# Performance work log

Measured on AMD Instinct MI355X. Metric: run time of the kernel, lower is better.

The kernel has to match this reference:

```python
import jax, jax.numpy as jnp
import numpy as np

NEG_VALUE = -1e7
EPS = 1e-13


def setup_inputs() -> dict:
    key = jax.random.key(0)
    k1, k2, k3, k4, k5 = jax.random.split(key, 5)
    B, C_L, Q_L, D2 = 32, 2048, 256, 256  # D2 = 2*model_dim
    context = jax.random.normal(k1, (B, C_L, D2), dtype=jnp.float32)
    query = jax.random.normal(k2, (B, Q_L, D2), dtype=jnp.float32)
    context_mask = (jax.random.uniform(k3, (B, C_L)) > 0.1).astype(jnp.float32)
    query_mask = (jax.random.uniform(k4, (B, Q_L)) > 0.1).astype(jnp.float32)
    # Linear(6*model_dim, 1, bias=False) weight, flattened to [3*D2]
    W = jax.random.normal(k5, (3 * D2,), dtype=jnp.float32) * 0.05
    return {"context": context, "context_mask": context_mask,
            "query": query, "query_mask": query_mask, "W": W}


def _masked_softmax(vector, mask):
    # claf / old-AllenNLP style: softmax(vector * mask) * mask, renormalized
    result = jax.nn.softmax(vector * mask, axis=-1) * mask
    return result / (result.sum(axis=-1, keepdims=True) + EPS)


def reference(context, context_mask, query, query_mask, W):
    c, q = context, query
    D2 = c.shape[-1]
    w_c, w_q, w_cq = W[:D2], W[D2:2 * D2], W[2 * D2:]
    # Decomposed similarity: S[b,i,j] = c_i.w_c + q_j.w_q + (c_i*q_j).w_cq
    # (same math as Linear over concat(c_aug, q_aug, c_aug*q_aug), no 6D blowup)
    S = (jnp.einsum('bcd,d->bc', c, w_c)[:, :, None]
         + jnp.einsum('bqd,d->bq', q, w_q)[:, None, :]
         + jnp.einsum('bcd,bqd->bcq', c * w_cq, q))  # [B, C_L, Q_L]

    qm = query_mask[:, None, :]  # [B, 1, Q_L]
    # add_masked_value: vector*mask + (1-mask)*value
    masked_S = S * qm + (1.0 - qm) * NEG_VALUE

    # C2Q: masked softmax over query dim, weighted sum of q
    attn_c2q = _masked_softmax(S, qm)                      # [B, C_L, Q_L]
    c2q = jnp.einsum('bcq,bqd->bcd', attn_c2q, q)           # [B, C_L, D2]

    # Q2C: max over query dim, masked softmax over context dim, weighted sum of c
    s_max = masked_S.max(axis=-1)                           # [B, C_L]
    attn_q2c = _masked_softmax(s_max, context_mask)         # [B, C_L]
    q2c = jnp.einsum('bc,bcd->bd', attn_q2c, c)             # [B, D2]

    G = jnp.concatenate(
        [c, c2q, c * c2q, c * q2c[:, None, :]], axis=-1)    # [B, C_L, 4*D2]
    return G
```

## Files before the change

### kernel.cpp

```cpp
#include <hip/hip_runtime.h>


#define CL 2048
#define QL 256
#define DD 256
#define TM 128
#define NEGV -1.0e7f

typedef short bs8 __attribute__((ext_vector_type(8)));
typedef float fx4 __attribute__((ext_vector_type(4)));

__device__ __forceinline__ short f2bf(float x) {
    unsigned u = __float_as_uint(x);
    unsigned r = (u + 0x7fffu + ((u >> 16) & 1u)) >> 16;
    return (short)r;
}
__device__ __forceinline__ float bf2f(short h) {
    return __uint_as_float(((unsigned)(unsigned short)h) << 16);
}
__device__ __forceinline__ void gl16(const short* g, short* l) {
    __builtin_amdgcn_global_load_lds(
        (const __attribute__((address_space(1))) void*)g,
        (__attribute__((address_space(3))) void*)l, 16, 0, 0);
}
#define LGKM0() asm volatile("s_waitcnt lgkmcnt(0)" ::: "memory")
#define VMC4()  asm volatile("s_waitcnt vmcnt(4)" ::: "memory")
#define VMC3()  asm volatile("s_waitcnt vmcnt(3)" ::: "memory")
#define VMC1()  asm volatile("s_waitcnt vmcnt(1)" ::: "memory")
#define VMC0()  asm volatile("s_waitcnt vmcnt(0)" ::: "memory")

__global__ void k0_split(const float* __restrict__ q, const float* __restrict__ W,
                         short* __restrict__ qh, short* __restrict__ qth,
                         float* __restrict__ sq) {
    __shared__ float lds[64][259];
    __shared__ float wq_l[256];
    int t = threadIdx.x, lane = t & 63, w = t >> 6;
    int b = blockIdx.y, cn = blockIdx.x;
    if (t < 64) *(fx4*)&wq_l[t * 4] = *(const fx4*)(W + 256 + t * 4);
    for (int r = 0; r < 64; ++r)
        lds[r][t] = q[((size_t)b * QL + cn * 64 + r) * DD + t];
    __syncthreads();
    for (int r = 0; r < 64; ++r) {
        size_t o = ((size_t)b * QL + cn * 64 + r) * DD + t;
        qh[o] = f2bf(lds[r][t]);
    }
    for (int dd = 0; dd < 64; ++dd) {
        int d = w * 64 + dd;
        size_t o = ((size_t)b * DD + d) * QL + cn * 64 + lane;
        qth[o] = f2bf(lds[lane][d]);
    }
    int r = t >> 2, qt = t & 3;
    float s = 0.0f;
    for (int i = 0; i < 64; ++i) {
        int colr = qt * 64 + ((i + r) & 63);
        s = fmaf(lds[r][colr], wq_l[colr], s);
    }
    s += __shfl_xor(s, 1, 64);
    s += __shfl_xor(s, 2, 64);
    if (qt == 0) sq[b * QL + cn * 64 + r] = s;
}

__global__ __launch_bounds__(1024, 4) void k1(
        const float* __restrict__ ctx, const float* __restrict__ qmask,
        const float* __restrict__ cmask,
        const short* __restrict__ qh, const short* __restrict__ qth,
        const float* __restrict__ sq, const float* __restrict__ W,
        float* __restrict__ G, float* __restrict__ q2cp,
        float* __restrict__ zup, float* __restrict__ zap) {
    __shared__ __align__(16) char SMEM[77312];
    short* Bc   = (short*)SMEM;
    short* Qt   = (short*)SMEM;
    float* pout = (float*)SMEM;
    short* Pb   = (short*)(SMEM + 32768);
    float* sq_l  = (float*)(SMEM + 67584);
    float* qm_l  = sq_l + 256;
    float* wcq_l = qm_l + 256;
    float* wc_l  = wcq_l + 256;
    float* sc_l  = wc_l + 256;
    float* redA  = sc_l + 128;
    float* redB  = redA + 512;
    float* er_l  = redB + 512;
    float* zar_l = er_l + 128;

    int t = threadIdx.x, lane = t & 63, wid = t >> 6;
    int wm = wid >> 1, wn = wid & 1;
    int l15 = lane & 15, lk = lane >> 4;
    int id = blockIdx.x;
    int xcd = id & 7, j = id >> 3;
    int b = xcd * 4 + (j >> 4);
    int bx = j & 15;
    int c0 = bx * TM;

    if (t < 256) sq_l[t] = sq[b * QL + t];
    else if (t < 512) qm_l[t - 256] = qmask[b * QL + (t - 256)];
    if (t < 64) *(fx4*)&wcq_l[t * 4] = *(const fx4*)(W + 512 + t * 4);
    else if (t < 128) *(fx4*)&wc_l[(t - 64) * 4] = *(const fx4*)(W + (t - 64) * 4);

    const short* qhb = qh + (size_t)b * QL * DD;
    const short* qtb = qth + (size_t)b * DD * QL;
    const float* ctxb = ctx + ((size_t)b * CL + c0) * DD;

    int srow = 16 * wid + (lane >> 2);
    int ssub = ((lane & 3) ^ ((srow >> 1) & 3)) << 3;

    auto stageB = [&](int p, int kk) {
        gl16(qhb + (size_t)srow * DD + kk * 32 + ssub,
             Bc + (p * 256 + 16 * wid) * 32);
    };
    auto stageQ = [&](int p, int s) {
        gl16(qtb + (size_t)srow * QL + s * 32 + ssub,
             Qt + (p * 256 + 16 * wid) * 32);
    };

    fx4 acc[8];
#pragma unroll
    for (int i = 0; i < 8; ++i) acc[i] = (fx4)0.0f;
    float scp = 0.0f;
    int arow = 16 * wm + l15;
    const float* aptr = ctxb + (size_t)arow * DD + lk * 8;
    float* g0ptr = G + ((size_t)b * CL + c0 + arow) * 1024 + lk * 8 + wn * 4;

    stageB(0, 0); stageB(1, 1);
    fx4 a0 = *(const fx4*)(aptr);
    fx4 a1 = *(const fx4*)(aptr + 4);
    __syncthreads();

#pragma unroll
    for (int kk = 0; kk < 8; ++kk) {
        int cur = kk % 3;
        fx4 n0 = a0, n1 = a1;
        if (kk < 7) {
            n0 = *(const fx4*)(aptr + (kk + 1) * 32);
            n1 = *(const fx4*)(aptr + (kk + 1) * 32 + 4);
        }
        fx4 w0 = *(const fx4*)&wcq_l[kk * 32 + lk * 8];
        fx4 w1 = *(const fx4*)&wcq_l[kk * 32 + lk * 8 + 4];
        fx4 v0 = *(const fx4*)&wc_l[kk * 32 + lk * 8];
        fx4 v1 = *(const fx4*)&wc_l[kk * 32 + lk * 8 + 4];
        scp += a0[0] * v0[0] + a0[1] * v0[1] + a0[2] * v0[2] + a0[3] * v0[3]
             + a1[0] * v1[0] + a1[1] * v1[1] + a1[2] * v1[2] + a1[3] * v1[3];
        bs8 Ah, Al;
#pragma unroll
        for (int i = 0; i < 4; ++i) {
            float a = a0[i] * w0[i];
            short h = f2bf(a); Ah[i] = h; Al[i] = f2bf(a - bf2f(h));
            float c = a1[i] * w1[i];
            short h2 = f2bf(c); Ah[4 + i] = h2; Al[4 + i] = f2bf(c - bf2f(h2));
        }
        __builtin_amdgcn_s_setprio(1);
#pragma unroll
        for (int nt = 0; nt < 8; ++nt) {
            int col = 128 * wn + 16 * nt + l15;
            int ko = ((lk ^ ((col >> 1) & 3)) << 3);
            bs8 Bh = *(const bs8*)&Bc[(cur * 256 + col) * 32 + ko];
            acc[nt] = __builtin_amdgcn_mfma_f32_16x16x32_bf16(Ah, Bh, acc[nt], 0, 0, 0);
            acc[nt] = __builtin_amdgcn_mfma_f32_16x16x32_bf16(Al, Bh, acc[nt], 0, 0, 0);
        }
        __builtin_amdgcn_s_setprio(0);
        if (kk == 7) break;
        LGKM0();
        if (kk < 6) { stageB((kk + 2) % 3, kk + 2); VMC4(); }
        else        { VMC3(); }
        __builtin_amdgcn_s_barrier();
        *(fx4*)(g0ptr + kk * 32) = wn ? a1 : a0;
        a0 = n0; a1 = n1;
    }
    *(fx4*)(g0ptr + 7 * 32) = wn ? a1 : a0;
    scp += __shfl_xor(scp, 16, 64);
    scp += __shfl_xor(scp, 32, 64);
    if (lk == 0 && wn == 0) sc_l[arow] = scp;
    __syncthreads();
    stageQ(0, 0); stageQ(1, 1);

    float mall[4], mu[4], scv[4];
#pragma unroll
    for (int j2 = 0; j2 < 4; ++j2) {
        mall[j2] = -3.0e38f; mu[j2] = -3.0e38f;
        scv[j2] = sc_l[16 * wm + 4 * lk + j2];
    }
#pragma unroll
    for (int nt = 0; nt < 8; ++nt) {
        int col = 128 * wn + 16 * nt + l15;
        float sqv = sq_l[col], qmv = qm_l[col];
#pragma unroll
        for (int j2 = 0; j2 < 4; ++j2) {
            float S = acc[nt][j2] + scv[j2] + sqv;
            float xm = S * qmv;
            float ms = (qmv != 0.0f) ? S : NEGV;
            acc[nt][j2] = xm;
            mall[j2] = fmaxf(mall[j2], xm);
            mu[j2]   = fmaxf(mu[j2], ms);
        }
    }
#pragma unroll
    for (int s = 1; s <= 8; s <<= 1)
#pragma unroll
        for (int j2 = 0; j2 < 4; ++j2) {
            mall[j2] = fmaxf(mall[j2], __shfl_xor(mall[j2], s, 64));
            mu[j2]   = fmaxf(mu[j2],   __shfl_xor(mu[j2], s, 64));
        }
    if (l15 == 0)
#pragma unroll
        for (int j2 = 0; j2 < 4; ++j2) {
            redA[wn * 256 + 0 * 128 + 16 * wm + 4 * lk + j2] = mall[j2];
            redA[wn * 256 + 1 * 128 + 16 * wm + 4 * lk + j2] = mu[j2];
        }
    __syncthreads();
#pragma unroll
    for (int j2 = 0; j2 < 4; ++j2) {
        int row = 16 * wm + 4 * lk + j2;
        mall[j2] = fmaxf(redA[row], redA[256 + row]);
        mu[j2]   = fmaxf(redA[128 + row], redA[384 + row]);
    }
    if (wn == 0 && l15 == 0)
#pragma unroll
        for (int j2 = 0; j2 < 4; ++j2) {
            int row = 16 * wm + 4 * lk + j2;
            float cm = cmask[(size_t)b * CL + c0 + row];
            float e  = (cm != 0.0f) ? __expf(mu[j2] - 32.0f) : 0.0f;
            er_l[row]  = e;
            zar_l[row] = (cm != 0.0f) ? e : 1.2664166e-14f;
        }

    float zal[4] = {0, 0, 0, 0}, zum[4] = {0, 0, 0, 0};
#pragma unroll
    for (int nt = 0; nt < 8; ++nt) {
        int col = 128 * wn + 16 * nt + l15;
        float qmv = qm_l[col];
#pragma unroll
        for (int j2 = 0; j2 < 4; ++j2) {
            float e = __expf(acc[nt][j2] - mall[j2]);
            acc[nt][j2] = e * qmv;
            zal[j2] += e;
            zum[j2] += acc[nt][j2];
        }
    }
#pragma unroll
    for (int s = 1; s <= 8; s <<= 1)
#pragma unroll
        for (int j2 = 0; j2 < 4; ++j2) {
            zal[j2] += __shfl_xor(zal[j2], s, 64);
            zum[j2] += __shfl_xor(zum[j2], s, 64);
        }
    if (l15 == 0)
#pragma unroll
        for (int j2 = 0; j2 < 4; ++j2) {
            redB[wn * 256 + 0 * 128 + 16 * wm + 4 * lk + j2] = zal[j2];
            redB[wn * 256 + 1 * 128 + 16 * wm + 4 * lk + j2] = zum[j2];
        }
    __syncthreads();
    float inv[4];
#pragma unroll
    for (int j2 = 0; j2 < 4; ++j2) {
        int row = 16 * wm + 4 * lk + j2;
        float Za = redB[row] + redB[256 + row];
        float Zu = redB[128 + row] + redB[384 + row];
        inv[j2] = 1.0f / (Zu + 1e-13f * Za);
    }
    __syncthreads();

    int prow = 16 * wm + l15;
    if (wn == 0) {
#pragma unroll
        for (int nt = 0; nt < 8; ++nt)
#pragma unroll
            for (int j2 = 0; j2 < 4; ++j2)
                Pb[(16 * wm + 4 * lk + j2) * 136 + 16 * nt + l15] =
                    f2bf(acc[nt][j2] * inv[j2]);
    }
    __syncthreads();

    fx4 acc2[8];
#pragma unroll
    for (int i = 0; i < 8; ++i) acc2[i] = (fx4)0.0f;
#pragma unroll
    for (int s = 0; s < 8; ++s) {
        int cur = s & 1, k2 = s & 3;
        bs8 Ph = *(const bs8*)&Pb[prow * 136 + k2 * 32 + lk * 8];
        __builtin_amdgcn_s_setprio(1);
#pragma unroll
        for (int nt = 0; nt < 8; ++nt) {
            int d = 128 * wn + 16 * nt + l15;
            int ko = ((lk ^ ((d >> 1) & 3)) << 3);
            bs8 Bh = *(const bs8*)&Qt[(cur * 256 + d) * 32 + ko];
            acc2[nt] = __builtin_amdgcn_mfma_f32_16x16x32_bf16(Ph, Bh, acc2[nt], 0, 0, 0);
        }
        __builtin_amdgcn_s_setprio(0);
        if (s == 7) break;
        LGKM0();
        __builtin_amdgcn_s_barrier();
        if (s < 6) stageQ(cur, s + 2);
        if (s == 3) {
            if (wn == 1) {
#pragma unroll
                for (int nt = 0; nt < 8; ++nt)
#pragma unroll
                    for (int j2 = 0; j2 < 4; ++j2)
                        Pb[(16 * wm + 4 * lk + j2) * 136 + 16 * nt + l15] =
                            f2bf(acc[nt][j2] * inv[j2]);
            }
            LGKM0();
        }
        if (s < 6) { VMC1(); } else { VMC0(); }
        __builtin_amdgcn_s_barrier();
    }
    __syncthreads();

    int erow = t >> 3, eu = t & 7;
    for (int h = 0; h < 2; ++h) {
        if (h) __syncthreads();
        if (wn == h) {
#pragma unroll
            for (int nt = 0; nt < 8; ++nt)
#pragma unroll
                for (int j2 = 0; j2 < 4; ++j2) {
                    int row = 16 * wm + 4 * lk + j2;
                    int col = 16 * nt + l15;
                    pout[row * 128 + (col ^ ((row & 7) << 2))] = acc2[nt][j2];
                }
        }
        __syncthreads();
        size_t grow = (size_t)b * CL + c0 + erow;
#pragma unroll
        for (int kkl = 0; kkl < 4; ++kkl) {
            int colL = kkl * 32 + eu * 4;
            fx4 cv = *(const fx4*)&ctxb[(size_t)erow * DD + 128 * h + colL];
            fx4 pv = *(const fx4*)&pout[erow * 128 + (colL ^ ((erow & 7) << 2))];
            float* gb = G + grow * 1024;
            __builtin_nontemporal_store(pv, (fx4*)&gb[256 + 128 * h + colL]);
            fx4 p2; p2[0] = cv[0] * pv[0]; p2[1] = cv[1] * pv[1];
            p2[2] = cv[2] * pv[2]; p2[3] = cv[3] * pv[3];
            __builtin_nontemporal_store(p2, (fx4*)&gb[512 + 128 * h + colL]);
        }
    }

    int colq = t & 255, rh = t >> 8;
    float accq = 0.0f;
#pragma unroll 8
    for (int r = rh * 32; r < rh * 32 + 32; ++r)
        accq = fmaf(er_l[r], ctxb[(size_t)r * DD + colq], accq);
    __builtin_nontemporal_store(
        accq, &q2cp[(((size_t)b * 16 + bx) * 4 + rh) * 256 + colq]);
    if (t < 128) {
        float e = er_l[t], za = zar_l[t];
#pragma unroll
        for (int sft = 32; sft >= 1; sft >>= 1) {
            e  += __shfl_xor(e, sft, 64);
            za += __shfl_xor(za, sft, 64);
        }
        if (lane == 0) {
            zup[b * 32 + bx * 2 + wid] = e;
            zap[b * 32 + bx * 2 + wid] = za;
        }
    }
}

__global__ void k2c(const float* __restrict__ q2cp, const float* __restrict__ zup,
                    const float* __restrict__ zap, float* __restrict__ q2c) {
    __shared__ float part[4][256];
    int t = threadIdx.x, b = blockIdx.x;
    int col = t & 255, g = t >> 8;
    float s = 0.0f;
#pragma unroll 4
    for (int p = g * 16; p < g * 16 + 16; ++p)
        s += q2cp[((size_t)b * 64 + p) * 256 + col];
    part[g][col] = s;
    __syncthreads();
    if (t < 256) {
        float zu = 0.0f, za = 0.0f;
        for (int i = 0; i < 32; ++i) { zu += zup[b * 32 + i]; za += zap[b * 32 + i]; }
        float inv = 1.0f / (zu + 1e-13f * za);
        q2c[b * DD + t] = (part[0][t] + part[1][t] + part[2][t] + part[3][t]) * inv;
    }
}

__global__ void k3(const float* __restrict__ ctx, const float* __restrict__ q2c,
                   float* __restrict__ G) {
    __shared__ fx4 qv[64];
    int t = threadIdx.x, lane = t & 63, w = t >> 6;
    int b = blockIdx.y;
    if (t < 64) qv[t] = ((const fx4*)q2c)[b * 64 + t];
    __syncthreads();
    int c0 = blockIdx.x * 64;
    fx4 q4 = qv[lane];
#pragma unroll 4
    for (int r = w; r < 64; r += 4) {
        size_t grow = (size_t)b * CL + c0 + r;
        fx4 cv = __builtin_nontemporal_load(((const fx4*)ctx) + grow * 64 + lane);
        fx4 o;
        o[0] = cv[0] * q4[0]; o[1] = cv[1] * q4[1];
        o[2] = cv[2] * q4[2]; o[3] = cv[3] * q4[3];
        __builtin_nontemporal_store(o, ((fx4*)G) + grow * 256 + 192 + lane);
    }
}

extern "C" void kernel_launch(void* const* d_in, const int* in_sizes, int n_in,
                              void* d_out, int out_size, void* d_ws, size_t ws_size,
                              hipStream_t stream) {
    const float* ctx   = (const float*)d_in[0];
    const float* cmask = (const float*)d_in[1];
    const float* q     = (const float*)d_in[2];
    const float* qmask = (const float*)d_in[3];
    const float* W     = (const float*)d_in[4];
    float* G = (float*)d_out;

    char* ws = (char*)d_ws;
    if (ws_size < (size_t)10559488) return;
    short* qh  = (short*)(ws);
    short* qth = (short*)(ws + 4194304);
    float* sq   = (float*)(ws + 8388608);
    float* q2cp = (float*)(ws + 8421376);
    float* zup  = (float*)(ws + 10518528);
    float* zap  = (float*)(ws + 10522624);
    float* q2cv = (float*)(ws + 10526720);

    k0_split<<<dim3(4, 32), dim3(256), 0, stream>>>(q, W, qh, qth, sq);
    k1<<<dim3(512), dim3(1024), 0, stream>>>(ctx, qmask, cmask, qh, qth,
                                             sq, W, G, q2cp, zup, zap);
    k2c<<<dim3(32), dim3(1024), 0, stream>>>(q2cp, zup, zap, q2cv);
    k3<<<dim3(32, 32), dim3(256), 0, stream>>>(ctx, q2cv, G);
}
```

Before: 147.1 us.

## Fuse q2c reduction and final G block into k1 via grid-wide counter and flags

Moves the q2c partial sums earlier in k1. The last block of each batch, detected with an atomic counter, finishes the q2c reduction and publishes it through a release flag. Every block spins on that flag and then writes the c*q2c quarter of G itself, which removes the k2c and k3 launches and the second read of context. The bf16 hi/lo split also switches from round-to-nearest to plain truncation, which is cheaper but slightly less accurate. The spin-wait assumes all 16 blocks of a batch are co-resident, so it risks deadlock if they are not.

Result: slower. 355.7 us (+141.8%).

```diff
diff --git a/kernel.cpp b/kernel.cpp
--- a/kernel.cpp
+++ b/kernel.cpp
@@ -66,8 +66,10 @@
         const short* __restrict__ qh, const short* __restrict__ qth,
         const float* __restrict__ sq, const float* __restrict__ W,
         float* __restrict__ G, float* __restrict__ q2cp,
-        float* __restrict__ zup, float* __restrict__ zap) {
-    __shared__ __align__(16) char SMEM[77312];
+        float* __restrict__ zup, float* __restrict__ zap,
+        float* __restrict__ q2cF, int* __restrict__ cnt,
+        int* __restrict__ flags) {
+    __shared__ __align__(16) char SMEM[77440];
     short* Bc   = (short*)SMEM;
     short* Qt   = (short*)SMEM;
     float* pout = (float*)SMEM;
@@ -81,6 +83,7 @@
     float* redB  = redA + 512;
     float* er_l  = redB + 512;
     float* zar_l = er_l + 128;
+    int*   fin_l = (int*)(zar_l + 128);
 
     int t = threadIdx.x, lane = t & 63, wid = t >> 6;
     int wm = wid >> 1, wn = wid & 1;
@@ -143,9 +146,15 @@
 #pragma unroll
         for (int i = 0; i < 4; ++i) {
             float a = a0[i] * w0[i];
-            short h = f2bf(a); Ah[i] = h; Al[i] = f2bf(a - bf2f(h));
+            unsigned ua = __float_as_uint(a);
+            Ah[i] = (short)(ua >> 16);
+            float lo = a - __uint_as_float(ua & 0xffff0000u);
+            Al[i] = (short)(__float_as_uint(lo) >> 16);
             float c = a1[i] * w1[i];
-            short h2 = f2bf(c); Ah[4 + i] = h2; Al[4 + i] = f2bf(c - bf2f(h2));
+            unsigned uc = __float_as_uint(c);
+            Ah[4 + i] = (short)(uc >> 16);
+            float lo2 = c - __uint_as_float(uc & 0xffff0000u);
+            Al[4 + i] = (short)(__float_as_uint(lo2) >> 16);
         }
         __builtin_amdgcn_s_setprio(1);
 #pragma unroll
@@ -257,7 +266,59 @@
         float Zu = redB[128 + row] + redB[384 + row];
         inv[j2] = 1.0f / (Zu + 1e-13f * Za);
     }
-    __syncthreads();
+
+    {
+        int colq = t & 255, rh = t >> 8;
+        float accq = 0.0f;
+#pragma unroll 8
+        for (int r = rh * 32; r < rh * 32 + 32; ++r)
+            accq = fmaf(er_l[r], ctxb[(size_t)r * DD + colq], accq);
+        q2cp[(((size_t)b * 16 + bx) * 4 + rh) * 256 + colq] = accq;
+        if (t < 128) {
+            float e = er_l[t], za = zar_l[t];
+#pragma unroll
+            for (int sft = 32; sft >= 1; sft >>= 1) {
+                e  += __shfl_xor(e, sft, 64);
+                za += __shfl_xor(za, sft, 64);
+            }
+            if (lane == 0) {
+                zup[b * 32 + bx * 2 + wid] = e;
+                zap[b * 32 + bx * 2 + wid] = za;
+            }
+        }
+    }
+    __syncthreads();
+    if (t == 0) {
+        __threadfence();
+        fin_l[0] = (atomicAdd(cnt + b, 1) == 15);
+    }
+    __syncthreads();
+    if (fin_l[0]) {
+        __threadfence();
+        float* part = redA;
+        int col = t & 255, g = t >> 8;
+        float s = 0.0f;
+#pragma unroll 4
+        for (int p = g * 16; p < g * 16 + 16; ++p)
+            s += q2cp[((size_t)b * 64 + p) * 256 + col];
+        part[g * 256 + col] = s;
+        __syncthreads();
+        if (t < 256) {
+            float zu = 0.0f, za = 0.0f;
+            for (int i = 0; i < 32; ++i) {
+                zu += zup[b * 32 + i]; za += zap[b * 32 + i];
+            }
+            float invz = 1.0f / (zu + 1e-13f * za);
+            q2cF[b * 256 + t] =
+                (part[t] + part[256 + t] + part[512 + t] + part[768 + t]) * invz;
+        }
+        __syncthreads();
+        if (t == 0) {
+            __threadfence();
+            __hip_atomic_store(flags + b, 1, __ATOMIC_RELEASE,
+                               __HIP_MEMORY_SCOPE_AGENT);
+        }
+    }
 
     int prow = 16 * wm + l15;
     if (wn == 0) {
@@ -306,6 +367,16 @@
     }
     __syncthreads();
 
+    if (t == 0) {
+        while (__hip_atomic_load(flags + b, __ATOMIC_ACQUIRE,
+                                 __HIP_MEMORY_SCOPE_AGENT) == 0)
+            __builtin_amdgcn_s_sleep(2);
+    }
+    __syncthreads();
+    __threadfence();
+    if (t < 256) sq_l[t] = q2cF[b * 256 + t];
+    __syncthreads();
+
     int erow = t >> 3, eu = t & 7;
     for (int h = 0; h < 2; ++h) {
         if (h) __syncthreads();
@@ -326,71 +397,16 @@
             int colL = kkl * 32 + eu * 4;
             fx4 cv = *(const fx4*)&ctxb[(size_t)erow * DD + 128 * h + colL];
             fx4 pv = *(const fx4*)&pout[erow * 128 + (colL ^ ((erow & 7) << 2))];
+            fx4 q4 = *(const fx4*)&sq_l[128 * h + colL];
             float* gb = G + grow * 1024;
             __builtin_nontemporal_store(pv, (fx4*)&gb[256 + 128 * h + colL]);
             fx4 p2; p2[0] = cv[0] * pv[0]; p2[1] = cv[1] * pv[1];
             p2[2] = cv[2] * pv[2]; p2[3] = cv[3] * pv[3];
             __builtin_nontemporal_store(p2, (fx4*)&gb[512 + 128 * h + colL]);
-        }
-    }
-
-    int colq = t & 255, rh = t >> 8;
-    float accq = 0.0f;
-#pragma unroll 8
-    for (int r = rh * 32; r < rh * 32 + 32; ++r)
-        accq = fmaf(er_l[r], ctxb[(size_t)r * DD + colq], accq);
-    __builtin_nontemporal_store(
-        accq, &q2cp[(((size_t)b * 16 + bx) * 4 + rh) * 256 + colq]);
-    if (t < 128) {
-        float e = er_l[t], za = zar_l[t];
-#pragma unroll
-        for (int sft = 32; sft >= 1; sft >>= 1) {
-            e  += __shfl_xor(e, sft, 64);
-            za += __shfl_xor(za, sft, 64);
-        }
-        if (lane == 0) {
-            zup[b * 32 + bx * 2 + wid] = e;
-            zap[b * 32 + bx * 2 + wid] = za;
-        }
-    }
-}
-
-__global__ void k2c(const float* __restrict__ q2cp, const float* __restrict__ zup,
-                    const float* __restrict__ zap, float* __restrict__ q2c) {
-    __shared__ float part[4][256];
-    int t = threadIdx.x, b = blockIdx.x;
-    int col = t & 255, g = t >> 8;
-    float s = 0.0f;
-#pragma unroll 4
-    for (int p = g * 16; p < g * 16 + 16; ++p)
-        s += q2cp[((size_t)b * 64 + p) * 256 + col];
-    part[g][col] = s;
-    __syncthreads();
-    if (t < 256) {
-        float zu = 0.0f, za = 0.0f;
-        for (int i = 0; i < 32; ++i) { zu += zup[b * 32 + i]; za += zap[b * 32 + i]; }
-        float inv = 1.0f / (zu + 1e-13f * za);
-        q2c[b * DD + t] = (part[0][t] + part[1][t] + part[2][t] + part[3][t]) * inv;
-    }
-}
-
-__global__ void k3(const float* __restrict__ ctx, const float* __restrict__ q2c,
-                   float* __restrict__ G) {
-    __shared__ fx4 qv[64];
-    int t = threadIdx.x, lane = t & 63, w = t >> 6;
-    int b = blockIdx.y;
-    if (t < 64) qv[t] = ((const fx4*)q2c)[b * 64 + t];
-    __syncthreads();
-    int c0 = blockIdx.x * 64;
-    fx4 q4 = qv[lane];
-#pragma unroll 4
-    for (int r = w; r < 64; r += 4) {
-        size_t grow = (size_t)b * CL + c0 + r;
-        fx4 cv = __builtin_nontemporal_load(((const fx4*)ctx) + grow * 64 + lane);
-        fx4 o;
-        o[0] = cv[0] * q4[0]; o[1] = cv[1] * q4[1];
-        o[2] = cv[2] * q4[2]; o[3] = cv[3] * q4[3];
-        __builtin_nontemporal_store(o, ((fx4*)G) + grow * 256 + 192 + lane);
+            fx4 p3; p3[0] = cv[0] * q4[0]; p3[1] = cv[1] * q4[1];
+            p3[2] = cv[2] * q4[2]; p3[3] = cv[3] * q4[3];
+            __builtin_nontemporal_store(p3, (fx4*)&gb[768 + 128 * h + colL]);
+        }
     }
 }
 
@@ -405,18 +421,20 @@
     float* G = (float*)d_out;
 
     char* ws = (char*)d_ws;
-    if (ws_size < (size_t)10559488) return;
+    if (ws_size < (size_t)10559744) return;
     short* qh  = (short*)(ws);
     short* qth = (short*)(ws + 4194304);
     float* sq   = (float*)(ws + 8388608);
     float* q2cp = (float*)(ws + 8421376);
     float* zup  = (float*)(ws + 10518528);
     float* zap  = (float*)(ws + 10522624);
-    float* q2cv = (float*)(ws + 10526720);
-
+    float* q2cF = (float*)(ws + 10526720);
+    int*   cnt   = (int*)(ws + 10559488);
+    int*   flags = (int*)(ws + 10559616);
+
+    hipMemsetAsync(cnt, 0, 256, stream);
     k0_split<<<dim3(4, 32), dim3(256), 0, stream>>>(q, W, qh, qth, sq);
     k1<<<dim3(512), dim3(1024), 0, stream>>>(ctx, qmask, cmask, qh, qth,
-                                             sq, W, G, q2cp, zup, zap);
-    k2c<<<dim3(32), dim3(1024), 0, stream>>>(q2cp, zup, zap, q2cv);
-    k3<<<dim3(32, 32), dim3(256), 0, stream>>>(ctx, q2cv, G);
-}
+                                             sq, W, G, q2cp, zup, zap,
+                                             q2cF, cnt, flags);
+}
```
